# Optimization experiments

Measured on AMD Instinct MI355X. Metric: run time of the kernel, lower is better.

The kernel has to match this reference:

```python
import jax, jax.numpy as jnp
import numpy as np

N_NODES = 100000
N_EDGES = 3200000


def setup_inputs() -> dict:
    key = jax.random.key(0)
    ks = jax.random.split(key, 20)
    x = jax.random.normal(ks[0], (N_NODES, 3), dtype=jnp.float32)
    edge_index = jax.random.randint(ks[1], (2, N_EDGES), 0, N_NODES, dtype=jnp.int64)

    def w(k, shape, fan_in):
        return jax.random.normal(k, shape, dtype=jnp.float32) * (1.0 / np.sqrt(fan_in))

    return {
        "x": x, "edge_index": edge_index,
        # layer 1: in=3, out=16, heads=2
        "W1": w(ks[2], (3, 32), 3), "a_src1": w(ks[3], (2, 16), 16), "a_dst1": w(ks[4], (2, 16), 16), "b1": jnp.zeros((32,), jnp.float32),
        # layer 2: in=32, out=16, heads=2
        "W2": w(ks[5], (32, 32), 32), "a_src2": w(ks[6], (2, 16), 16), "a_dst2": w(ks[7], (2, 16), 16), "b2": jnp.zeros((32,), jnp.float32),
        # layer 3: in=32, out=16, heads=1
        "W3": w(ks[8], (32, 16), 32), "a_src3": w(ks[9], (1, 16), 16), "a_dst3": w(ks[10], (1, 16), 16), "b3": jnp.zeros((16,), jnp.float32),
        # output linear 16 -> 1
        "Wout": w(ks[11], (16, 1), 16), "bout": jnp.zeros((1,), jnp.float32),
    }


def gat_layer(x, src, dst, W, a_src, a_dst, b, heads, ch, n):
    # h: [N, H, C]
    h = (x @ W).reshape(n, heads, ch)
    alpha_src = jnp.sum(h * a_src[None], axis=-1)  # [N, H]
    alpha_dst = jnp.sum(h * a_dst[None], axis=-1)  # [N, H]
    e = jax.nn.leaky_relu(alpha_src[src] + alpha_dst[dst], 0.2)  # [E, H]
    # segment softmax over incoming edges of each dst node
    m = jax.ops.segment_max(e, dst, num_segments=n)
    m = jnp.where(jnp.isfinite(m), m, 0.0)
    ex = jnp.exp(e - jax.lax.stop_gradient(m)[dst])
    s = jax.ops.segment_sum(ex, dst, num_segments=n)
    alpha = ex / (s[dst] + 1e-16)  # [E, H]
    out = jax.ops.segment_sum(h[src] * alpha[:, :, None], dst, num_segments=n)  # [N, H, C]
    return out.reshape(n, heads * ch) + b


def reference(x, edge_index, W1, a_src1, a_dst1, b1, W2, a_src2, a_dst2, b2,
              W3, a_src3, a_dst3, b3, Wout, bout):
    n = x.shape[0]
    loops = jnp.arange(n, dtype=edge_index.dtype)
    src = jnp.concatenate([edge_index[0], loops])  # PyG add_self_loops=True
    dst = jnp.concatenate([edge_index[1], loops])
    h = jax.nn.elu(gat_layer(x, src, dst, W1, a_src1, a_dst1, b1, 2, 16, n))
    h = jax.nn.elu(gat_layer(h, src, dst, W2, a_src2, a_dst2, b2, 2, 16, n))
    h = jax.nn.elu(gat_layer(h, src, dst, W3, a_src3, a_dst3, b3, 1, 16, n))
    embeddings = h
    out = jax.nn.sigmoid(h @ Wout + bout)
    return out, embeddings
```

## Files before the change

kernel.cpp:

```cpp
#include <hip/hip_runtime.h>
#include <hip/hip_fp16.h>
#include <math.h>

#define TPB 256
#define PMAX 128
#define PSH 10
#define PW  1024
#define CHUNK 2048
#define KPT 8
#define PCAP 49152
#define PCSTR 16

__device__ __forceinline__ float leaky02(float x) { return x > 0.f ? x : 0.2f * x; }
__device__ __forceinline__ float eluf(float x) { return x > 0.f ? x : (__expf(x) - 1.f); }


__global__ void zero_kernel(int* __restrict__ p, int n) {
  int i = blockIdx.x * blockDim.x + threadIdx.x;
  if (i < n) p[i] = 0;
}

__global__ __launch_bounds__(256) void scatter_kernel(const int* __restrict__ src,
                                                      const int* __restrict__ dst,
                                                      int E, int n,
                                                      int* __restrict__ pcursor,
                                                      unsigned* __restrict__ pstage) {
  __shared__ int lcnt[4][PMAX];
  __shared__ int ltot[PMAX];
  __shared__ int lscan[PMAX];
  __shared__ int lbase[PMAX];
  __shared__ int wtot;
  __shared__ unsigned slab[CHUNK];
  int t = threadIdx.x;
  int wid = t >> 6;
  int lane = t & 63;
  int Etot = E + n;
  int c0 = blockIdx.x * CHUNK;
  if (c0 >= Etot) return;
  int c1 = min(c0 + CHUNK, Etot);
  for (int j = t; j < 4 * PMAX; j += TPB) ((int*)lcnt)[j] = 0;

  int dd[KPT], ss[KPT];
  bool vv[KPT];
#pragma unroll
  for (int k = 0; k < KPT; ++k) {
    int idx = c0 + t + k * TPB;
    vv[k] = idx < c1;
    if (vv[k]) {
      if (idx < E) { ss[k] = src[idx]; dd[k] = dst[idx]; }
      else         { ss[k] = dd[k] = idx - E; }
    } else { ss[k] = 0; dd[k] = 0; }
  }
  __syncthreads();
#pragma unroll
  for (int k = 0; k < KPT; ++k)
    if (vv[k]) atomicAdd(&lcnt[wid][dd[k] >> PSH], 1);
  __syncthreads();
  int tot = 0, x = 0;
  if (t < PMAX) {
    int a0 = lcnt[0][t], a1 = lcnt[1][t], a2 = lcnt[2][t], a3 = lcnt[3][t];
    tot = a0 + a1 + a2 + a3;
    ltot[t] = tot;
    lcnt[0][t] = 0; lcnt[1][t] = a0; lcnt[2][t] = a0 + a1; lcnt[3][t] = a0 + a1 + a2;
    x = tot;
#pragma unroll
    for (int off = 1; off < 64; off <<= 1) {
      int u = __shfl_up(x, off);
      if (lane >= off) x += u;
    }
    if (t == 63) wtot = x;
  }
  __syncthreads();
  if (t < PMAX) {
    lscan[t] = x - tot + ((t >= 64) ? wtot : 0);
    lbase[t] = tot ? atomicAdd(&pcursor[t * PCSTR], tot) : 0;
  }
  __syncthreads();
#pragma unroll
  for (int k = 0; k < KPT; ++k) {
    if (vv[k]) {
      int p = dd[k] >> PSH;
      int sub = atomicAdd(&lcnt[wid][p], 1);
      slab[lscan[p] + sub] = ((unsigned)ss[k] << PSH) | (unsigned)(dd[k] & (PW - 1));
    }
  }
  __syncthreads();
  for (int p = wid; p < PMAX; p += 4) {
    int cnt = ltot[p];
    int s = lscan[p];
    size_t b = (size_t)p * PCAP + lbase[p];
    for (int j = lane; j < cnt; j += 64)
      pstage[b + j] = slab[s + j];
  }
}

__global__ __launch_bounds__(1024) void build_csr_kernel(const unsigned* __restrict__ pstage,
                                                         const int* __restrict__ pcursor,
                                                         int nvtx,
                                                         int* __restrict__ rowptr,
                                                         int* __restrict__ csr_src) {
  __shared__ int ssum[PMAX];
  __shared__ int lhist[PW];
  __shared__ int lcur[PW];
  int t = threadIdx.x;
  int lane = t & 63;
  int wid = t >> 6;
  int p = blockIdx.x;
  size_t rbase = (size_t)p * PCAP;
  if (t < PMAX) ssum[t] = pcursor[t * PCSTR];
  lhist[t] = 0;
  __syncthreads();
  for (int off = 1; off < PMAX; off <<= 1) {
    int a = 0;
    if (t < PMAX && t >= off) a = ssum[t - off];
    __syncthreads();
    if (t < PMAX) ssum[t] += a;
    __syncthreads();
  }
  int cnt = pcursor[p * PCSTR];
  int wbase = ssum[p] - cnt;
  int nodebase = p << PSH;
  for (int i = t; i < cnt; i += 4096) {
    unsigned w[4]; bool vv[4];
#pragma unroll
    for (int k = 0; k < 4; ++k) {
      int j = i + k * 1024;
      vv[k] = j < cnt;
      w[k] = vv[k] ? pstage[rbase + j] : 0u;
    }
#pragma unroll
    for (int k = 0; k < 4; ++k)
      if (vv[k]) atomicAdd(&lhist[w[k] & (PW - 1)], 1);
  }
  __syncthreads();
  int v = lhist[t];
  int x = v;
#pragma unroll
  for (int off = 1; off < 64; off <<= 1) {
    int u = __shfl_up(x, off);
    if (lane >= off) x += u;
  }
  if (lane == 63) lcur[wid] = x;
  __syncthreads();
  if (t < 16) {
    int wsum = lcur[t];
    int y = wsum;
#pragma unroll
    for (int off = 1; off < 16; off <<= 1) {
      int u = __shfl_up(y, off);
      if (t >= off) y += u;
    }
    lcur[t] = y - wsum;
  }
  __syncthreads();
  int acc = wbase + x + lcur[wid] - v;
  __syncthreads();
  lcur[t] = acc;
  int node = nodebase + t;
  if (node < nvtx) rowptr[node] = acc;
  __syncthreads();
  for (int i = t; i < cnt; i += 4096) {
    unsigned w[4]; bool vv[4];
#pragma unroll
    for (int k = 0; k < 4; ++k) {
      int j = i + k * 1024;
      vv[k] = j < cnt;
      w[k] = vv[k] ? pstage[rbase + j] : 0u;
    }
#pragma unroll
    for (int k = 0; k < 4; ++k) {
      if (vv[k]) {
        int pos = atomicAdd(&lcur[w[k] & (PW - 1)], 1);
        csr_src[pos] = (int)(w[k] >> PSH);
      }
    }
  }
  if (p == (int)gridDim.x - 1 && t == 0) rowptr[nvtx] = wbase + cnt;
}


template<int IN, int OUT, int H>
__global__ void transform_kernel(const float* __restrict__ x, const float* __restrict__ W,
                                 const float* __restrict__ a_src, const float* __restrict__ a_dst,
                                 __half* __restrict__ h, float* __restrict__ asrc,
                                 float* __restrict__ adst, int n) {
  __shared__ float sW[IN * OUT];
  __shared__ float sa[2 * OUT];
  for (int i = threadIdx.x; i < IN * OUT; i += blockDim.x) sW[i] = W[i];
  if (threadIdx.x < OUT) {
    sa[threadIdx.x] = a_src[threadIdx.x];
    sa[OUT + threadIdx.x] = a_dst[threadIdx.x];
  }
  __syncthreads();
  int i = blockIdx.x * blockDim.x + threadIdx.x;
  if (i >= n) return;
  float xv[IN];
#pragma unroll
  for (int k = 0; k < IN; k++) xv[k] = x[(size_t)i * IN + k];
  float hv[OUT];
#pragma unroll
  for (int j = 0; j < OUT; j++) {
    float acc = 0.f;
#pragma unroll
    for (int k = 0; k < IN; k++) acc += xv[k] * sW[k * OUT + j];
    hv[j] = acc;
  }
#pragma unroll
  for (int j = 0; j < OUT; j += 2)
    ((__half2*)h)[((size_t)i * OUT + j) >> 1] = __floats2half2_rn(hv[j], hv[j + 1]);
#pragma unroll
  for (int hh = 0; hh < H; hh++) {
    float as = 0.f, ad = 0.f;
#pragma unroll
    for (int c = 0; c < 16; c++) {
      as += hv[hh * 16 + c] * sa[hh * 16 + c];
      ad += hv[hh * 16 + c] * sa[OUT + hh * 16 + c];
    }
    asrc[i * H + hh] = as;
    adst[i * H + hh] = ad;
  }
}


__global__ __launch_bounds__(256) void node_gat12(
    const int* __restrict__ rowptr,
    const int* __restrict__ csr_src,
    const float* __restrict__ asrc,
    const float* __restrict__ adst,
    const __half* __restrict__ hfeat,
    const float* __restrict__ bias,
    float* __restrict__ outb,
    int n) {
  __shared__ float4 s_e[4][64];
  int wid = threadIdx.x >> 6;
  int lane = threadIdx.x & 63;
  int i = (blockIdx.x * blockDim.x + threadIdx.x) >> 6;
  if (i >= n) return;
  int start = rowptr[i];
  int d = rowptr[i + 1] - start;
  float ad0 = adst[i * 2 + 0];
  float ad1 = adst[i * 2 + 1];
  const uint2* hfp = (const uint2*)hfeat;
  const float2* asrc2 = (const float2*)asrc;
  int g = lane >> 3;
  int q = lane & 7;
  const float2* sp = (const float2*)(&s_e[wid][0]) + (q >> 2);
  float4 acc = make_float4(0.f, 0.f, 0.f, 0.f);
  float sl0 = 0.f, sl1 = 0.f;

  if (d <= 64) {
    int sidx8 = 0;
    float w0 = 0.f, w1 = 0.f;
    if (lane < d) {
      int sidx = csr_src[start + lane];
      sidx8 = sidx << 3;
      float2 av = asrc2[sidx];
      w0 = __expf(leaky02(av.x + ad0));
      w1 = __expf(leaky02(av.y + ad1));
    }
    sl0 = w0; sl1 = w1;
    s_e[wid][lane] = make_float4(__int_as_float(sidx8), w0, __int_as_float(sidx8), w1);
    float2 p[8];
#pragma unroll
    for (int it = 0; it < 8; ++it) p[it] = sp[2 * (g + it * 8)];
    uint2 hv[8];
#pragma unroll
    for (int it = 0; it < 8; ++it) hv[it] = hfp[__float_as_int(p[it].x) + q];
#pragma unroll
    for (int it = 0; it < 8; ++it) {
      float2 fa = __half22float2(*(const __half2*)&hv[it].x);
      float2 fb = __half22float2(*(const __half2*)&hv[it].y);
      float w = p[it].y;
      acc.x += w * fa.x; acc.y += w * fa.y;
      acc.z += w * fb.x; acc.w += w * fb.y;
    }
  } else {
    for (int base = 0; base < d; base += 64) {
      int k = base + lane;
      int sidx8 = 0;
      float w0 = 0.f, w1 = 0.f;
      if (k < d) {
        int sidx = csr_src[start + k];
        sidx8 = sidx << 3;
        float2 av = asrc2[sidx];
        w0 = __expf(leaky02(av.x + ad0));
        w1 = __expf(leaky02(av.y + ad1));
        sl0 += w0; sl1 += w1;
      }
      s_e[wid][lane] = make_float4(__int_as_float(sidx8), w0, __int_as_float(sidx8), w1);
      float2 p[8];
#pragma unroll
      for (int it = 0; it < 8; ++it) p[it] = sp[2 * (g + it * 8)];
      uint2 hv[8];
#pragma unroll
      for (int it = 0; it < 8; ++it) hv[it] = hfp[__float_as_int(p[it].x) + q];
#pragma unroll
      for (int it = 0; it < 8; ++it) {
        float2 fa = __half22float2(*(const __half2*)&hv[it].x);
        float2 fb = __half22float2(*(const __half2*)&hv[it].y);
        float w = p[it].y;
        acc.x += w * fa.x; acc.y += w * fa.y;
        acc.z += w * fb.x; acc.w += w * fb.y;
      }
    }
  }

#pragma unroll
  for (int off = 32; off >= 1; off >>= 1) {
    sl0 += __shfl_xor(sl0, off);
    sl1 += __shfl_xor(sl1, off);
  }
#pragma unroll
  for (int off = 8; off <= 32; off <<= 1) {
    acc.x += __shfl_xor(acc.x, off);
    acc.y += __shfl_xor(acc.y, off);
    acc.z += __shfl_xor(acc.z, off);
    acc.w += __shfl_xor(acc.w, off);
  }
  if (lane < 8) {
    float inv = 1.f / (((lane >= 4) ? sl1 : sl0) + 1e-16f);
    float4 bv = ((const float4*)bias)[lane];
    float4 o;
    o.x = eluf(acc.x * inv + bv.x);
    o.y = eluf(acc.y * inv + bv.y);
    o.z = eluf(acc.z * inv + bv.z);
    o.w = eluf(acc.w * inv + bv.w);
    ((float4*)outb)[(size_t)i * 8 + lane] = o;
  }
}

__global__ __launch_bounds__(256) void node_gat3(
    const int* __restrict__ rowptr,
    const int* __restrict__ csr_src,
    const float* __restrict__ asrc,
    const float* __restrict__ adst,
    const __half* __restrict__ hfeat,
    const float* __restrict__ b3,
    const float* __restrict__ Wout,
    const float* __restrict__ bout,
    float* __restrict__ out,
    int n) {
  __shared__ float2 s_hw[4][64];
  int wid = threadIdx.x >> 6;
  int lane = threadIdx.x & 63;
  int i = (blockIdx.x * blockDim.x + threadIdx.x) >> 6;
  if (i >= n) return;
  int start = rowptr[i];
  int d = rowptr[i + 1] - start;
  float ad0 = adst[i];
  const uint2* hfp = (const uint2*)hfeat;
  int g = lane >> 2;
  int q = lane & 3;
  const float2* sp = s_hw[wid];
  float4 acc = make_float4(0.f, 0.f, 0.f, 0.f);
  float sl = 0.f;

  if (d <= 64) {
    int sidx4 = 0;
    float w0 = 0.f;
    if (lane < d) {
      int sidx = csr_src[start + lane];
      sidx4 = sidx << 2;
      w0 = __expf(leaky02(asrc[sidx] + ad0));
    }
    sl = w0;
    s_hw[wid][lane] = make_float2(__int_as_float(sidx4), w0);
    float2 p[4];
#pragma unroll
    for (int it = 0; it < 4; ++it) p[it] = sp[g + it * 16];
    uint2 hv[4];
#pragma unroll
    for (int it = 0; it < 4; ++it) hv[it] = hfp[__float_as_int(p[it].x) + q];
#pragma unroll
    for (int it = 0; it < 4; ++it) {
      float2 fa = __half22float2(*(const __half2*)&hv[it].x);
      float2 fb = __half22float2(*(const __half2*)&hv[it].y);
      float w = p[it].y;
      acc.x += w * fa.x; acc.y += w * fa.y;
      acc.z += w * fb.x; acc.w += w * fb.y;
    }
  } else {
    for (int base = 0; base < d; base += 64) {
      int k = base + lane;
      int sidx4 = 0;
      float w0 = 0.f;
      if (k < d) {
        int sidx = csr_src[start + k];
        sidx4 = sidx << 2;
        w0 = __expf(leaky02(asrc[sidx] + ad0));
        sl += w0;
      }
      s_hw[wid][lane] = make_float2(__int_as_float(sidx4), w0);
      float2 p[4];
#pragma unroll
      for (int it = 0; it < 4; ++it) p[it] = sp[g + it * 16];
      uint2 hv[4];
#pragma unroll
      for (int it = 0; it < 4; ++it) hv[it] = hfp[__float_as_int(p[it].x) + q];
#pragma unroll
      for (int it = 0; it < 4; ++it) {
        float2 fa = __half22float2(*(const __half2*)&hv[it].x);
        float2 fb = __half22float2(*(const __half2*)&hv[it].y);
        float w = p[it].y;
        acc.x += w * fa.x; acc.y += w * fa.y;
        acc.z += w * fb.x; acc.w += w * fb.y;
      }
    }
  }

#pragma unroll
  for (int off = 32; off >= 1; off >>= 1) sl += __shfl_xor(sl, off);
#pragma unroll
  for (int off = 4; off <= 32; off <<= 1) {
    acc.x += __shfl_xor(acc.x, off);
    acc.y += __shfl_xor(acc.y, off);
    acc.z += __shfl_xor(acc.z, off);
    acc.w += __shfl_xor(acc.w, off);
  }
  float z = 0.f;
  if (lane < 4) {
    float inv = 1.f / (sl + 1e-16f);
    float4 bv = ((const float4*)b3)[lane];
    float4 wv = ((const float4*)Wout)[lane];
    float4 o;
    o.x = eluf(acc.x * inv + bv.x);
    o.y = eluf(acc.y * inv + bv.y);
    o.z = eluf(acc.z * inv + bv.z);
    o.w = eluf(acc.w * inv + bv.w);
    ((float4*)(out + n))[(size_t)i * 4 + lane] = o;
    z = o.x * wv.x + o.y * wv.y + o.z * wv.z + o.w * wv.w;
  }
  z += __shfl_xor(z, 1);
  z += __shfl_xor(z, 2);
  if (lane == 0) out[i] = 1.f / (1.f + __expf(-(z + bout[0])));
}


extern "C" void kernel_launch(void* const* d_in, const int* in_sizes, int n_in,
                              void* d_out, int out_size, void* d_ws, size_t ws_size,
                              hipStream_t stream) {
  const float* x    = (const float*)d_in[0];
  const int*   ei   = (const int*)d_in[1];
  const float* W1   = (const float*)d_in[2];
  const float* as1  = (const float*)d_in[3];
  const float* ad1  = (const float*)d_in[4];
  const float* b1   = (const float*)d_in[5];
  const float* W2   = (const float*)d_in[6];
  const float* as2  = (const float*)d_in[7];
  const float* ad2  = (const float*)d_in[8];
  const float* b2   = (const float*)d_in[9];
  const float* W3   = (const float*)d_in[10];
  const float* as3  = (const float*)d_in[11];
  const float* ad3  = (const float*)d_in[12];
  const float* b3   = (const float*)d_in[13];
  const float* Wout = (const float*)d_in[14];
  const float* bout = (const float*)d_in[15];
  float* out = (float*)d_out;

  const int n = in_sizes[0] / 3;
  const int E = in_sizes[1] / 2;
  const int Etot = E + n;
  const int* src = ei;
  const int* dst = ei + E;
  const int nbC = (Etot + CHUNK - 1) / CHUNK;
  const int NP = ((n - 1) >> PSH) + 1;

  float* ws = (float*)d_ws;
  float* bufH = ws;
  float* bufX = bufH + (size_t)n * 32;
  float* asrc = bufX + (size_t)n * 32;
  float* adst = asrc + (size_t)n * 2;
  int* rowptr  = (int*)(adst + (size_t)n * 2);
  int* pcursor = rowptr + n + 1;
  int* csr_src = pcursor + PMAX * PCSTR;
  unsigned* pstage = (unsigned*)ws;
  __half* hH = (__half*)bufH;

  const int nbN = (n + TPB - 1) / TPB;
  const int nbW = (n + 3) / 4;

  zero_kernel<<<(PMAX * PCSTR + TPB - 1) / TPB, TPB, 0, stream>>>(pcursor, PMAX * PCSTR);
  scatter_kernel<<<nbC, TPB, 0, stream>>>(src, dst, E, n, pcursor, pstage);
  build_csr_kernel<<<NP, 1024, 0, stream>>>(pstage, pcursor, n, rowptr, csr_src);

  transform_kernel<3, 32, 2><<<nbN, TPB, 0, stream>>>(x, W1, as1, ad1, hH, asrc, adst, n);
  node_gat12<<<nbW, TPB, 0, stream>>>(rowptr, csr_src, asrc, adst, hH, b1, bufX, n);

  transform_kernel<32, 32, 2><<<nbN, TPB, 0, stream>>>(bufX, W2, as2, ad2, hH, asrc, adst, n);
  node_gat12<<<nbW, TPB, 0, stream>>>(rowptr, csr_src, asrc, adst, hH, b2, bufX, n);

  transform_kernel<32, 16, 1><<<nbN, TPB, 0, stream>>>(bufX, W3, as3, ad3, hH, asrc, adst, n);
  node_gat3<<<nbW, TPB, 0, stream>>>(rowptr, csr_src, asrc, adst, hH, b3, Wout, bout, out, n);
}
```

Baseline: 360.3 us.

## Fuse next-layer linear transform and attention logits into GAT aggregation kernel

The aggregation kernel for layers 1 and 2 now applies the next layer's weight matrix and attention vectors to each node's output. It writes fp16 features and the src/dst logits straight from shared memory, so the separate transform kernels for layers 2 and 3 go away. This removes two launches and the fp32 round trip of the intermediate node features. In exchange each block loads the weights into shared memory, and most lanes sit idle during the small per-node matvec. The workspace is relaid out into ping-pong half buffers, and PCAP is reduced to fit.

Result: slower. 376.1 us (+4.4%).

```diff
diff --git a/kernel.cpp b/kernel.cpp
--- a/kernel.cpp
+++ b/kernel.cpp
@@ -8,7 +8,7 @@
 #define PW  1024
 #define CHUNK 2048
 #define KPT 8
-#define PCAP 49152
+#define PCAP 38912
 #define PCSTR 16
 
 __device__ __forceinline__ float leaky02(float x) { return x > 0.f ? x : 0.2f * x; }
@@ -222,26 +222,39 @@
 }
 
 
-__global__ __launch_bounds__(256) void node_gat12(
+template<int OUT2, int H2>
+__global__ __launch_bounds__(256) void node_gat12_t(
     const int* __restrict__ rowptr,
     const int* __restrict__ csr_src,
     const float* __restrict__ asrc,
     const float* __restrict__ adst,
     const __half* __restrict__ hfeat,
     const float* __restrict__ bias,
-    float* __restrict__ outb,
+    const float* __restrict__ W2,
+    const float* __restrict__ a_src2,
+    const float* __restrict__ a_dst2,
+    __half* __restrict__ h2out,
+    float* __restrict__ asrc2,
+    float* __restrict__ adst2,
     int n) {
   __shared__ float4 s_e[4][64];
-  int wid = threadIdx.x >> 6;
-  int lane = threadIdx.x & 63;
-  int i = (blockIdx.x * blockDim.x + threadIdx.x) >> 6;
+  __shared__ float  s_o[4][32];
+  __shared__ float  sW[32 * OUT2];
+  __shared__ float  sa2[2 * OUT2];
+  int t = threadIdx.x;
+  int wid = t >> 6;
+  int lane = t & 63;
+  for (int jj = t; jj < 32 * OUT2; jj += TPB) sW[jj] = W2[jj];
+  if (t < OUT2) { sa2[t] = a_src2[t]; sa2[OUT2 + t] = a_dst2[t]; }
+  __syncthreads();
+  int i = (blockIdx.x * blockDim.x + t) >> 6;
   if (i >= n) return;
   int start = rowptr[i];
   int d = rowptr[i + 1] - start;
   float ad0 = adst[i * 2 + 0];
   float ad1 = adst[i * 2 + 1];
   const uint2* hfp = (const uint2*)hfeat;
-  const float2* asrc2 = (const float2*)asrc;
+  const float2* asrc_2 = (const float2*)asrc;
   int g = lane >> 3;
   int q = lane & 7;
   const float2* sp = (const float2*)(&s_e[wid][0]) + (q >> 2);
@@ -254,7 +267,7 @@
     if (lane < d) {
       int sidx = csr_src[start + lane];
       sidx8 = sidx << 3;
-      float2 av = asrc2[sidx];
+      float2 av = asrc_2[sidx];
       w0 = __expf(leaky02(av.x + ad0));
       w1 = __expf(leaky02(av.y + ad1));
     }
@@ -282,7 +295,7 @@
       if (k < d) {
         int sidx = csr_src[start + k];
         sidx8 = sidx << 3;
-        float2 av = asrc2[sidx];
+        float2 av = asrc_2[sidx];
         w0 = __expf(leaky02(av.x + ad0));
         w1 = __expf(leaky02(av.y + ad1));
         sl0 += w0; sl1 += w1;
@@ -325,9 +338,29 @@
     o.y = eluf(acc.y * inv + bv.y);
     o.z = eluf(acc.z * inv + bv.z);
     o.w = eluf(acc.w * inv + bv.w);
-    ((float4*)outb)[(size_t)i * 8 + lane] = o;
-  }
-}
+    ((float4*)s_o[wid])[lane] = o;
+  }
+  float h2 = 0.f;
+  if (lane < OUT2) {
+    const float* so = s_o[wid];
+#pragma unroll
+    for (int k = 0; k < 32; ++k) h2 += so[k] * sW[k * OUT2 + lane];
+    h2out[(size_t)i * OUT2 + lane] = __float2half_rn(h2);
+  }
+  float ps = 0.f, pd = 0.f;
+  if (lane < OUT2) { ps = h2 * sa2[lane]; pd = h2 * sa2[OUT2 + lane]; }
+#pragma unroll
+  for (int off = 1; off <= 8; off <<= 1) {
+    ps += __shfl_xor(ps, off);
+    pd += __shfl_xor(pd, off);
+  }
+  if (lane < OUT2 && (lane & 15) == 0) {
+    int hh = lane >> 4;
+    asrc2[(size_t)i * H2 + hh] = ps;
+    adst2[(size_t)i * H2 + hh] = pd;
+  }
+}
+
 
 __global__ __launch_bounds__(256) void node_gat3(
     const int* __restrict__ rowptr,
@@ -466,15 +499,19 @@
   const int NP = ((n - 1) >> PSH) + 1;
 
   float* ws = (float*)d_ws;
-  float* bufH = ws;
-  float* bufX = bufH + (size_t)n * 32;
-  float* asrc = bufX + (size_t)n * 32;
-  float* adst = asrc + (size_t)n * 2;
-  int* rowptr  = (int*)(adst + (size_t)n * 2);
+  __half* hA = (__half*)ws;
+  __half* hB = (__half*)(ws + (size_t)n * 16);
+  __half* hC = (__half*)(ws + (size_t)n * 32);
+  float* asrcA = ws + (size_t)n * 40;
+  float* adstA = asrcA + (size_t)n * 2;
+  float* asrcB = adstA + (size_t)n * 2;
+  float* adstB = asrcB + (size_t)n * 2;
+  float* asrcC = adstB + (size_t)n * 2;
+  float* adstC = asrcC + (size_t)n;
+  int* rowptr  = (int*)(adstC + (size_t)n);
   int* pcursor = rowptr + n + 1;
   int* csr_src = pcursor + PMAX * PCSTR;
   unsigned* pstage = (unsigned*)ws;
-  __half* hH = (__half*)bufH;
 
   const int nbN = (n + TPB - 1) / TPB;
   const int nbW = (n + 3) / 4;
@@ -483,12 +520,10 @@
   scatter_kernel<<<nbC, TPB, 0, stream>>>(src, dst, E, n, pcursor, pstage);
   build_csr_kernel<<<NP, 1024, 0, stream>>>(pstage, pcursor, n, rowptr, csr_src);
 
-  transform_kernel<3, 32, 2><<<nbN, TPB, 0, stream>>>(x, W1, as1, ad1, hH, asrc, adst, n);
-  node_gat12<<<nbW, TPB, 0, stream>>>(rowptr, csr_src, asrc, adst, hH, b1, bufX, n);
-
-  transform_kernel<32, 32, 2><<<nbN, TPB, 0, stream>>>(bufX, W2, as2, ad2, hH, asrc, adst, n);
-  node_gat12<<<nbW, TPB, 0, stream>>>(rowptr, csr_src, asrc, adst, hH, b2, bufX, n);
-
-  transform_kernel<32, 16, 1><<<nbN, TPB, 0, stream>>>(bufX, W3, as3, ad3, hH, asrc, adst, n);
-  node_gat3<<<nbW, TPB, 0, stream>>>(rowptr, csr_src, asrc, adst, hH, b3, Wout, bout, out, n);
-}
+  transform_kernel<3, 32, 2><<<nbN, TPB, 0, stream>>>(x, W1, as1, ad1, hA, asrcA, adstA, n);
+  node_gat12_t<32, 2><<<nbW, TPB, 0, stream>>>(rowptr, csr_src, asrcA, adstA, hA, b1,
+                                               W2, as2, ad2, hB, asrcB, adstB, n);
+  node_gat12_t<16, 1><<<nbW, TPB, 0, stream>>>(rowptr, csr_src, asrcB, adstB, hB, b2,
+                                               W3, as3, ad3, hC, asrcC, adstC, n);
+  node_gat3<<<nbW, TPB, 0, stream>>>(rowptr, csr_src, asrcC, adstC, hC, b3, Wout, bout, out, n);
+}
```
